# Kernel tuning notes

Hardware: AMD Instinct MI355X
Metric: run time of the kernel (lower is better)

Reference implementation:

```python
import jax, jax.numpy as jnp
import numpy as np
from jax import lax

K = 5          # kernel_size
OC = 8         # out_num_capsules
OD = 32        # out_dims


def setup_inputs() -> dict:
    key = jax.random.key(0)
    k1, k2, k3 = jax.random.split(key, 3)
    u = jax.random.normal(k1, (4, 4, 16, 128, 128), jnp.float32)            # [B, in_caps, in_dims, H, W]
    W = jax.random.normal(k2, (4, OC * OD, 16, K, K), jnp.float32) * 0.05    # per-capsule Conv2d weights (OIHW)
    bias = jax.random.normal(k3, (4, OC * OD), jnp.float32) * 0.05
    return {"u": u, "W": W, "bias": bias}


def _squash(p):
    # p: [..., out_dims]
    sq = jnp.sum(p * p, axis=-1, keepdims=True)
    return sq / (1.0 + sq) * p / jnp.sqrt(sq + 1e-9)


def reference(u, W, bias):
    B, ic, _, H, Wd = u.shape

    def conv_one(x, w, b):  # x:[B,in_dims,H,W] w:[OC*OD,in_dims,K,K]
        y = lax.conv_general_dilated(x, w, (1, 1), [(2, 2), (2, 2)],
                                     dimension_numbers=("NCHW", "OIHW", "NCHW"))
        return y + b[None, :, None, None]

    # per-capsule conv, vmapped over the in_capsule axis -> [B, ic, OC*OD, H, W]
    u_hat = jax.vmap(conv_one, in_axes=(1, 0, 0), out_axes=1)(u, W, bias)
    # -> [B, ic, H, W, OC, OD] (matches torch reshape + transpose_(1,3).transpose_(2,4))
    u_hat = u_hat.reshape(B, ic, OC, OD, H, Wd).transpose(0, 1, 4, 5, 2, 3)

    # Routing logits b start at zero. NOTE: in the source, the update `b_t_list_`
    # is a dead store (never assigned back), so b stays zero for all iterations
    # and every routing iteration produces the identical v; one effective pass.
    b_r = jnp.zeros((B, OC, H, Wd), u.dtype)
    # windowed max (torch max_pool2d pads with -inf; k=5, pad=2 == SAME)
    b_max = lax.reduce_window(b_r, -jnp.inf, lax.max, (1, 1, K, K), (1, 1, 1, 1), "SAME")
    b_max = jnp.max(b_max, axis=1, keepdims=True)                 # [B,1,H,W]
    c = jnp.exp(b_r - b_max)                                      # [B,OC,H,W]
    # conv2d_same with an all-ones (1, OC, K, K) kernel == channel-sum then SAME window-sum
    sum_c = lax.reduce_window(jnp.sum(c, axis=1, keepdims=True), 0.0, lax.add,
                              (1, 1, K, K), (1, 1, 1, 1), "SAME")  # [B,1,H,W]
    r = (c / sum_c).transpose(0, 2, 3, 1)[..., None]              # [B,H,W,OC,1]

    # r is identical for every input capsule (b==0), so fold the capsule sum
    p = jnp.sum(r[:, None] * u_hat, axis=1)                       # [B,H,W,OC,OD]
    v = _squash(p)
    # final v.transpose_(1,3).transpose_(2,4) -> [B, OC, OD, H, W]
    return v.transpose(0, 3, 4, 1, 2)
```

## Files before the change

### kernel.cpp

```cpp
#include <hip/hip_runtime.h>
#include <math.h>

typedef __attribute__((ext_vector_type(8))) __bf16 b16x8;
typedef __attribute__((ext_vector_type(4))) float f32x4;

#define GLDS(gp, lp) __builtin_amdgcn_global_load_lds(                         \
    (const __attribute__((address_space(1))) unsigned int*)(gp),               \
    (__attribute__((address_space(3))) unsigned int*)(lp), 16, 0, 0)

#define WAIT_VM2()   asm volatile("s_waitcnt vmcnt(2)" ::: "memory")
#define WAIT_VM0()   asm volatile("s_waitcnt vmcnt(0)" ::: "memory")
#define BAR()        __builtin_amdgcn_s_barrier()

__device__ __forceinline__ unsigned short f2bf(float x) {
    unsigned int v = __float_as_uint(x);
    v += 0x7fffu + ((v >> 16) & 1u);
    return (unsigned short)(v >> 16);
}

__device__ __forceinline__ float red16(float x) {
    int v;
    v = __builtin_amdgcn_update_dpp(0, __float_as_int(x), 0xB1, 0xF, 0xF, true);
    x += __int_as_float(v);
    v = __builtin_amdgcn_update_dpp(0, __float_as_int(x), 0x4E, 0xF, 0xF, true);
    x += __int_as_float(v);
    v = __builtin_amdgcn_update_dpp(0, __float_as_int(x), 0x141, 0xF, 0xF, true);
    x += __int_as_float(v);
    v = __builtin_amdgcn_update_dpp(0, __float_as_int(x), 0x140, 0xF, 0xF, true);
    x += __int_as_float(v);
    return x;
}

__global__ __launch_bounds__(256) void repack_w(
    const float* __restrict__ Wt, const float* __restrict__ bias,
    unsigned short* __restrict__ wsw, float* __restrict__ wsb) {
    int idx = blockIdx.x * 256 + threadIdx.x;
    if (idx < 409600) {
        int j    = idx & 7;
        int cgp  = (idx >> 3) & 3;
        int o    = (idx >> 5) & 255;
        int l    = idx >> 13;
        int kh   = l % 5;
        int ks   = (l / 5) & 1;
        int kw   = l / 10;
        int tap  = kh * 5 + kw;
        int cg   = cgp ^ ((o >> 1) & 3);
        int cin  = ks * 32 + cg * 8 + j;
        int ic = cin >> 4, id = cin & 15;
        float w = Wt[((size_t)(ic * 256 + o) * 16 + id) * 25 + tap];
        wsw[idx] = f2bf(w);
    } else if (idx < 409856) {
        int o = idx - 409600;
        float s = 0.f;
        for (int ic = 0; ic < 4; ++ic) s += bias[ic * 256 + o];
        wsb[o] = s;
    }
}

__global__ __launch_bounds__(1024, 4) void caps_mfma(
    const float* __restrict__ u, const unsigned short* __restrict__ wsw,
    const float* __restrict__ wsb, float* __restrict__ out) {

    __shared__ __align__(16) unsigned short su_sh[25600];
    __shared__ __align__(16) unsigned short sw_sh[4][8192];

    const int tid  = threadIdx.x;
    const int lane = tid & 63;
    const int wid  = tid >> 6;
    const int wm   = wid >> 2;
    const int wn   = wid & 3;
    const int col  = lane & 15;
    const int cg   = lane >> 4;
    const int ybase = wm * 4;
    const int obase = wn * 64;

    const int bx  = blockIdx.x;
    const int b   = blockIdx.y;
    const int ty0 = (bx >> 3) * 16;
    const int tx0 = (bx & 7) * 16;

    int b_elem[4];
    #pragma unroll
    for (int fr = 0; fr < 4; ++fr) {
        int o = obase + fr * 16 + col;
        int cgp = cg ^ ((o >> 1) & 3);
        b_elem[fr] = o * 32 + cgp * 8;
    }

    int coffs[5];
    #pragma unroll
    for (int kw = 0; kw < 5; ++kw) {
        int hx = col + kw;
        coffs[kw] = hx * 32 + ((cg ^ ((hx >> 1) & 3)) * 8);
    }

    f32x4 acc[4][4];
    #pragma unroll
    for (int f = 0; f < 4; ++f)
        #pragma unroll
        for (int fr = 0; fr < 4; ++fr) acc[f][fr] = (f32x4)0.f;

    auto stage_u = [&](int half) {
        const float* up = u + ((size_t)b * 64 + half * 32) * 16384;
        unsigned short* dstp = su_sh + half * 12800;
        #pragma unroll 1
        for (int i = tid; i < 12800; i += 1024) {
            int c = i / 400;
            int s = i - c * 400;
            int hy = s / 20, hx = s - hy * 20;
            int gy = ty0 - 2 + hy, gx = tx0 - 2 + hx;
            float v = 0.f;
            if ((unsigned)gy < 128u && (unsigned)gx < 128u)
                v = up[(size_t)c * 16384 + gy * 128 + gx];
            int cgp = (c >> 3) ^ ((hx >> 1) & 3);
            dstp[(hy * 20 + hx) * 32 + cgp * 8 + (c & 7)] = f2bf(v);
        }
    };

    const char* wbase = ((const char*)wsw) + wid * 1024 + lane * 16;

    auto stage_unit = [&](int slot, int bufI) {
        const char* src = wbase + (size_t)slot * 16384;
        char* dst = ((char*)sw_sh) + bufI * 16384 + wid * 1024;
        GLDS(src, dst);
    };

    stage_unit(0, 0);
    stage_unit(1, 1);
    stage_unit(2, 2);
    stage_u(0);
    stage_u(1);
    __syncthreads();

    int l = 0;
    #pragma unroll 1
    for (int kw = 0; kw < 5; ++kw) {
        const int coff = coffs[kw];
        #pragma unroll 1
        for (int ks = 0; ks < 2; ++ks) {
            const unsigned short* apb = su_sh + ks * 12800 + ybase * 640 + coff;
            b16x8 aw[8];
            #pragma unroll
            for (int i = 0; i < 4; ++i)
                aw[i] = *reinterpret_cast<const b16x8*>(apb + i * 640);

            #pragma unroll
            for (int kh = 0; kh < 5; ++kh) {
                const int ln = (l + 3 > 49) ? 49 : l + 3;

                BAR();
                const unsigned short* swb = sw_sh[l & 3];
                b16x8 bf[4];
                #pragma unroll
                for (int fr = 0; fr < 4; ++fr)
                    bf[fr] = *reinterpret_cast<const b16x8*>(swb + b_elem[fr]);
                if (kh < 4)
                    aw[kh + 4] =
                        *reinterpret_cast<const b16x8*>(apb + (kh + 4) * 640);
                stage_unit(ln, (l + 3) & 3);

                __builtin_amdgcn_s_setprio(1);
                #pragma unroll
                for (int f = 0; f < 4; ++f)
                    #pragma unroll
                    for (int fr = 0; fr < 4; ++fr)
                        acc[f][fr] = __builtin_amdgcn_mfma_f32_16x16x32_bf16(
                            aw[kh + f], bf[fr], acc[f][fr], 0, 0, 0);
                __builtin_amdgcn_s_setprio(0);

                WAIT_VM2();
                ++l;
            }
        }
    }
    WAIT_VM0();

    float bsv[4];
    #pragma unroll
    for (int fr = 0; fr < 4; ++fr) bsv[fr] = wsb[obase + fr * 16 + col];

    const int xg = lane >> 4;
    #pragma unroll
    for (int f = 0; f < 4; ++f) {
        int h = ty0 + ybase + f;
        int rows = min(h + 2, 127) - max(h - 2, 0) + 1;
        #pragma unroll
        for (int p = 0; p < 2; ++p) {
            int oc = wn * 2 + p;
            float o0[4], o1[4];
            #pragma unroll
            for (int r = 0; r < 4; ++r) {
                int w = tx0 + xg * 4 + r;
                int colsv = min(w + 2, 127) - max(w - 2, 0) + 1;
                float rs = 1.0f / (8.0f * (float)(rows * colsv));
                float p0 = (acc[f][2 * p][r] + bsv[2 * p]) * rs;
                float p1 = (acc[f][2 * p + 1][r] + bsv[2 * p + 1]) * rs;
                o0[r] = p0; o1[r] = p1;
                float sv = red16(p0 * p0 + p1 * p1);
                float scale = sv / ((1.0f + sv) * sqrtf(sv + 1e-9f));
                o0[r] *= scale; o1[r] *= scale;
            }
            size_t base = ((size_t)((b * 8 + oc) * 32) + col) * 16384
                          + (size_t)h * 128 + tx0 + xg * 4;
            float4 v0 = make_float4(o0[0], o0[1], o0[2], o0[3]);
            float4 v1 = make_float4(o1[0], o1[1], o1[2], o1[3]);
            *reinterpret_cast<float4*>(out + base) = v0;
            *reinterpret_cast<float4*>(out + base + (size_t)16 * 16384) = v1;
        }
    }
}

extern "C" void kernel_launch(void* const* d_in, const int* in_sizes, int n_in,
                              void* d_out, int out_size, void* d_ws, size_t ws_size,
                              hipStream_t stream) {
    const float* u    = (const float*)d_in[0];
    const float* Wt   = (const float*)d_in[1];
    const float* bias = (const float*)d_in[2];
    unsigned short* wsw = (unsigned short*)d_ws;
    float* wsb = (float*)((char*)d_ws + 819200);

    repack_w<<<1601, 256, 0, stream>>>(Wt, bias, wsw, wsb);
    caps_mfma<<<dim3(64, 4), 1024, 0, stream>>>(u, wsw, wsb, (float*)d_out);
}
```

Before: 66.48 us.

## Load weight fragments directly from global into registers, dropping LDS staging

```diff
diff --git a/kernel.cpp b/kernel.cpp
--- a/kernel.cpp
+++ b/kernel.cpp
@@ -3,14 +3,6 @@
 
 typedef __attribute__((ext_vector_type(8))) __bf16 b16x8;
 typedef __attribute__((ext_vector_type(4))) float f32x4;
-
-#define GLDS(gp, lp) __builtin_amdgcn_global_load_lds(                         \
-    (const __attribute__((address_space(1))) unsigned int*)(gp),               \
-    (__attribute__((address_space(3))) unsigned int*)(lp), 16, 0, 0)
-
-#define WAIT_VM2()   asm volatile("s_waitcnt vmcnt(2)" ::: "memory")
-#define WAIT_VM0()   asm volatile("s_waitcnt vmcnt(0)" ::: "memory")
-#define BAR()        __builtin_amdgcn_s_barrier()
 
 __device__ __forceinline__ unsigned short f2bf(float x) {
     unsigned int v = __float_as_uint(x);
@@ -37,14 +29,17 @@
     int idx = blockIdx.x * 256 + threadIdx.x;
     if (idx < 409600) {
         int j    = idx & 7;
-        int cgp  = (idx >> 3) & 3;
-        int o    = (idx >> 5) & 255;
+        int lane = (idx >> 3) & 63;
+        int fr   = (idx >> 9) & 3;
+        int wn   = (idx >> 11) & 3;
         int l    = idx >> 13;
         int kh   = l % 5;
         int ks   = (l / 5) & 1;
         int kw   = l / 10;
         int tap  = kh * 5 + kw;
-        int cg   = cgp ^ ((o >> 1) & 3);
+        int col  = lane & 15;
+        int cg   = lane >> 4;
+        int o    = wn * 64 + fr * 16 + col;
         int cin  = ks * 32 + cg * 8 + j;
         int ic = cin >> 4, id = cin & 15;
         float w = Wt[((size_t)(ic * 256 + o) * 16 + id) * 25 + tap];
@@ -62,7 +57,6 @@
     const float* __restrict__ wsb, float* __restrict__ out) {
 
     __shared__ __align__(16) unsigned short su_sh[25600];
-    __shared__ __align__(16) unsigned short sw_sh[4][8192];
 
     const int tid  = threadIdx.x;
     const int lane = tid & 63;
@@ -78,14 +72,6 @@
     const int b   = blockIdx.y;
     const int ty0 = (bx >> 3) * 16;
     const int tx0 = (bx & 7) * 16;
-
-    int b_elem[4];
-    #pragma unroll
-    for (int fr = 0; fr < 4; ++fr) {
-        int o = obase + fr * 16 + col;
-        int cgp = cg ^ ((o >> 1) & 3);
-        b_elem[fr] = o * 32 + cgp * 8;
-    }
 
     int coffs[5];
     #pragma unroll
@@ -117,63 +103,58 @@
         }
     };
 
-    const char* wbase = ((const char*)wsw) + wid * 1024 + lane * 16;
-
-    auto stage_unit = [&](int slot, int bufI) {
-        const char* src = wbase + (size_t)slot * 16384;
-        char* dst = ((char*)sw_sh) + bufI * 16384 + wid * 1024;
-        GLDS(src, dst);
+    const char* wp0 = ((const char*)wsw) + wn * 4096 + lane * 16;
+    auto loadB = [&](int slot, b16x8* bf) {
+        const char* p = wp0 + (size_t)slot * 16384;
+        bf[0] = *reinterpret_cast<const b16x8*>(p);
+        bf[1] = *reinterpret_cast<const b16x8*>(p + 1024);
+        bf[2] = *reinterpret_cast<const b16x8*>(p + 2048);
+        bf[3] = *reinterpret_cast<const b16x8*>(p + 3072);
     };
 
-    stage_unit(0, 0);
-    stage_unit(1, 1);
-    stage_unit(2, 2);
+    b16x8 bfA[4], bfB[4];
+    loadB(0, bfA);
     stage_u(0);
     stage_u(1);
     __syncthreads();
 
-    int l = 0;
     #pragma unroll 1
-    for (int kw = 0; kw < 5; ++kw) {
-        const int coff = coffs[kw];
-        #pragma unroll 1
-        for (int ks = 0; ks < 2; ++ks) {
-            const unsigned short* apb = su_sh + ks * 12800 + ybase * 640 + coff;
-            b16x8 aw[8];
-            #pragma unroll
-            for (int i = 0; i < 4; ++i)
-                aw[i] = *reinterpret_cast<const b16x8*>(apb + i * 640);
-
-            #pragma unroll
-            for (int kh = 0; kh < 5; ++kh) {
-                const int ln = (l + 3 > 49) ? 49 : l + 3;
-
-                BAR();
-                const unsigned short* swb = sw_sh[l & 3];
-                b16x8 bf[4];
-                #pragma unroll
-                for (int fr = 0; fr < 4; ++fr)
-                    bf[fr] = *reinterpret_cast<const b16x8*>(swb + b_elem[fr]);
-                if (kh < 4)
-                    aw[kh + 4] =
-                        *reinterpret_cast<const b16x8*>(apb + (kh + 4) * 640);
-                stage_unit(ln, (l + 3) & 3);
-
-                __builtin_amdgcn_s_setprio(1);
-                #pragma unroll
-                for (int f = 0; f < 4; ++f)
-                    #pragma unroll
-                    for (int fr = 0; fr < 4; ++fr)
-                        acc[f][fr] = __builtin_amdgcn_mfma_f32_16x16x32_bf16(
-                            aw[kh + f], bf[fr], acc[f][fr], 0, 0, 0);
-                __builtin_amdgcn_s_setprio(0);
-
-                WAIT_VM2();
-                ++l;
-            }
+    for (int g = 0; g < 5; ++g) {
+        const unsigned short* base0 = su_sh + ybase * 640 + coffs[g];
+        const int l0 = g * 10;
+
+#define COMP(I, BF)                                                            \
+        {                                                                      \
+            const unsigned short* ap = base0 + ((I) / 5) * 12800               \
+                                             + ((I) % 5) * 640;                \
+            b16x8 a0 = *reinterpret_cast<const b16x8*>(ap);                    \
+            b16x8 a1 = *reinterpret_cast<const b16x8*>(ap + 640);              \
+            b16x8 a2 = *reinterpret_cast<const b16x8*>(ap + 1280);             \
+            b16x8 a3 = *reinterpret_cast<const b16x8*>(ap + 1920);             \
+            __builtin_amdgcn_s_setprio(1);                                     \
+            _Pragma("unroll")                                                  \
+            for (int fr = 0; fr < 4; ++fr) {                                   \
+                acc[0][fr] = __builtin_amdgcn_mfma_f32_16x16x32_bf16(          \
+                    a0, BF[fr], acc[0][fr], 0, 0, 0);                          \
+                acc[1][fr] = __builtin_amdgcn_mfma_f32_16x16x32_bf16(          \
+                    a1, BF[fr], acc[1][fr], 0, 0, 0);                          \
+                acc[2][fr] = __builtin_amdgcn_mfma_f32_16x16x32_bf16(          \
+                    a2, BF[fr], acc[2][fr], 0, 0, 0);                          \
+                acc[3][fr] = __builtin_amdgcn_mfma_f32_16x16x32_bf16(          \
+                    a3, BF[fr], acc[3][fr], 0, 0, 0);                          \
+            }                                                                  \
+            __builtin_amdgcn_s_setprio(0);                                     \
         }
-    }
-    WAIT_VM0();
+#define STEP2(I)                                                               \
+        loadB((l0 + (I) + 1 > 49) ? 49 : l0 + (I) + 1, bfB);                   \
+        COMP(I, bfA)                                                           \
+        loadB((l0 + (I) + 2 > 49) ? 49 : l0 + (I) + 2, bfA);                   \
+        COMP((I) + 1, bfB)
+
+        STEP2(0) STEP2(2) STEP2(4) STEP2(6) STEP2(8)
+#undef STEP2
+#undef COMP
+    }
 
     float bsv[4];
     #pragma unroll
```

After: 69.32 us. +4.3%, slower.
